# Optimization experiments

Measured on AMD Instinct MI355X. Metric: run time of the kernel, lower is better.

Reference implementation:

```python
import jax, jax.numpy as jnp
import numpy as np
import math

B, C, N, T = 16, 32, 500, 10
NH, DK = 8, 8
D = NH * DK  # 64
TT = 6       # tem_size after conv_temp1 (10->6)
EPS = 1e-5


def setup_inputs() -> dict:
    key = jax.random.key(0)
    ks = jax.random.split(key, 32)
    s = 0.05
    rn = lambda k, shp: jax.random.normal(k, shp, dtype=jnp.float32) * s
    return {
        "x": jax.random.normal(ks[0], (B, C, N, T), dtype=jnp.float32),
        "A": jax.random.uniform(ks[1], (N, N), dtype=jnp.float32) / N,
        "conv1_W": rn(ks[2], (32, 32)), "conv1_b": jnp.zeros((32,), jnp.float32),
        "te1_W": rn(ks[3], (64, 32)), "te1_b": jnp.zeros((64,), jnp.float32),
        "convq_W": rn(ks[4], (64, 64, 1, 3)), "convq_b": jnp.zeros((64,), jnp.float32),
        "convk_W": rn(ks[5], (64, 64, 1, 3)), "convk_b": jnp.zeros((64,), jnp.float32),
        "linv_W": rn(ks[6], (64, 64)), "linv_b": jnp.zeros((64,), jnp.float32),
        "lino_W": rn(ks[7], (64, 64)), "lino_b": jnp.zeros((64,), jnp.float32),
        "te2_W": rn(ks[8], (32, 64)), "te2_b": jnp.zeros((32,), jnp.float32),
        "mlp_W": rn(ks[9], (64, 160)), "mlp_b": jnp.zeros((64,), jnp.float32),
        "ct1_W": rn(ks[10], (6, 10)), "ct1_b": jnp.zeros((6,), jnp.float32),
        "tat_c1_W": rn(ks[11], (32,)), "tat_c2_W": rn(ks[12], (500,)),
        "tat_w": rn(ks[13], (500, 32)), "tat_b": jnp.zeros((6, 6), jnp.float32),
        "tat_v": rn(ks[14], (6, 6)),
        "bn1_g": jnp.ones((6,), jnp.float32), "bn1_b": jnp.zeros((6,), jnp.float32),
        "bn2_g": jnp.ones((32,), jnp.float32), "bn2_b": jnp.zeros((32,), jnp.float32),
    }


def _forward(x, A, conv1_W, conv1_b, te1_W, te1_b, convq_W, convq_b, convk_W, convk_b,
             linv_W, linv_b, lino_W, lino_b, te2_W, te2_b, mlp_W, mlp_b, ct1_W, ct1_b,
             tat_c1_W, tat_c2_W, tat_w, tat_b, tat_v, bn1_g, bn1_b, bn2_g, bn2_b):
    b, c, n, t = x.shape
    c1x1 = lambda z, W, bb: jnp.einsum('bchw,oc->bohw', z, W) + bb[None, :, None, None]
    residual = c1x1(x, conv1_W, conv1_b)                      # (B,32,N,T)
    h = c1x1(x, te1_W, te1_b)                                 # (B,64,N,T)
    # --- temporal-context multi-head self-attention (att bias is 0 in source due to bug) ---
    dn = ('NCHW', 'OIHW', 'NCHW')
    q = jax.lax.conv_general_dilated(h, convq_W, (1, 1), ((0, 0), (1, 1)), dimension_numbers=dn) + convq_b[None, :, None, None]
    k = jax.lax.conv_general_dilated(h, convk_W, (1, 1), ((0, 0), (1, 1)), dimension_numbers=dn) + convk_b[None, :, None, None]
    sh = lambda z: z.reshape(b, NH, DK, n, t).transpose(0, 3, 1, 4, 2)  # (B,N,h,T,dk)
    q, k = sh(q), sh(k)
    hp = h.transpose(0, 2, 3, 1)                              # (B,N,T,64)
    v = (hp @ linv_W.T + linv_b).reshape(b, n, t, NH, DK).transpose(0, 1, 3, 2, 4)
    p = jax.nn.softmax(jnp.einsum('bnhtd,bnhsd->bnhts', q, k) / math.sqrt(DK), axis=-1)
    o = jnp.einsum('bnhts,bnhsd->bnhtd', p, v).transpose(0, 1, 3, 2, 4).reshape(b, n, t, D)
    h = (o @ lino_W.T + lino_b).transpose(0, 3, 1, 2)         # (B,64,N,T)
    h = c1x1(h, te2_W, te2_b)                                 # (B,32,N,T)
    # --- multi_gcn_d: static adjacency diffusion + per-timestep attention adjacency ---
    co = h.shape[1]
    xt = h.transpose(0, 3, 2, 1)                              # (B,T,N,C)
    att = jax.nn.softmax(jnp.einsum('btnc,btmc->btnm', xt, xt) / math.sqrt(co), axis=-1)
    outs = [h]
    z = jnp.einsum('btvc,wv->btwc', xt, A); outs.append(z.transpose(0, 3, 2, 1))
    z = jnp.einsum('btvc,wv->btwc', z, A);  outs.append(z.transpose(0, 3, 2, 1))
    z = jnp.einsum('btvc,btwv->btwc', xt, att); outs.append(z.transpose(0, 3, 2, 1))
    z = jnp.einsum('btvc,btwv->btwc', z, att);  outs.append(z.transpose(0, 3, 2, 1))
    hc = c1x1(jnp.concatenate(outs, axis=1), mlp_W, mlp_b)    # (B,64,N,T)
    g = jnp.tanh(hc[:, :co]) * jax.nn.sigmoid(hc[:, co:])     # (B,32,N,10)
    # --- conv_temp1: 1x1 conv over the time axis, 10 -> 6 ---
    g = jnp.einsum('bcnt,st->bcns', g, ct1_W) + ct1_b[None, None, None, :]  # (B,32,N,6)
    # --- TATT_1 temporal attention coefficients ---
    f1 = jnp.einsum('bcnt,c->btn', g, tat_c1_W)               # (B,6,N)
    f2 = jnp.einsum('bcnt,n->bct', g, tat_c2_W)               # (B,32,6)
    logits = jax.nn.sigmoid(jnp.einsum('btn,nc,bcs->bts', f1, tat_w, f2) + tat_b)
    logits = jnp.einsum('pt,bts->bps', tat_v, logits)         # (B,6,6)
    lp = logits.transpose(0, 2, 1)
    mu = lp.mean((0, 2), keepdims=True); var = lp.var((0, 2), keepdims=True)
    lp = (lp - mu) / jnp.sqrt(var + EPS) * bn1_g[None, :, None] + bn1_b[None, :, None]
    coefs = jax.nn.softmax(lp.transpose(0, 2, 1), axis=-1)    # (B,6,6)
    Tc = coefs.transpose(0, 2, 1)
    xo = jnp.einsum('bcnl,blq->bcnq', g, Tc)                  # (B,32,N,6)
    xo = jnp.where(xo > 0, xo, 0.01 * xo) + residual[..., -xo.shape[-1]:]
    mu = xo.mean((0, 2, 3), keepdims=True); var = xo.var((0, 2, 3), keepdims=True)
    return (xo - mu) / jnp.sqrt(var + EPS) * bn2_g[None, :, None, None] + bn2_b[None, :, None, None]


def reference(x, A, conv1_W, conv1_b, te1_W, te1_b, convq_W, convq_b, convk_W, convk_b,
              linv_W, linv_b, lino_W, lino_b, te2_W, te2_b, mlp_W, mlp_b, ct1_W, ct1_b,
              tat_c1_W, tat_c2_W, tat_w, tat_b, tat_v, bn1_g, bn1_b, bn2_g, bn2_b):
    return _forward(x, A, conv1_W, conv1_b, te1_W, te1_b, convq_W, convq_b, convk_W, convk_b,
                    linv_W, linv_b, lino_W, lino_b, te2_W, te2_b, mlp_W, mlp_b, ct1_W, ct1_b,
                    tat_c1_W, tat_c2_W, tat_w, tat_b, tat_v, bn1_g, bn1_b, bn2_g, bn2_b)
```

## Files before the change

kernel.cpp:

```cpp
#include <hip/hip_runtime.h>

typedef unsigned short u16;
typedef unsigned int u32;

__device__ __forceinline__ float b2f(u16 v) { return __uint_as_float((u32)v << 16); }
__device__ __forceinline__ float lopart(u32 u) { return __uint_as_float(u << 16); }
__device__ __forceinline__ float hipart(u32 u) { return __uint_as_float(u & 0xffff0000u); }
__device__ __forceinline__ u16 f2b(float f) {
  u32 u = __float_as_uint(f);
  u32 r = u + 0x7fffu + ((u >> 16) & 1u);
  return (u16)(r >> 16);
}
__device__ __forceinline__ u32 pk2(float a, float b) {
  return (u32)f2b(a) | ((u32)f2b(b) << 16);
}
__device__ __forceinline__ u32 cvtpk(float lo, float hi) {
  u32 r;
  asm("v_cvt_pk_bf16_f32 %0, %1, %2" : "=v"(r) : "v"(lo), "v"(hi));
  return r;
}

struct Ptrs { const void* p[29]; };

typedef __attribute__((ext_vector_type(8))) short short8;
typedef __attribute__((ext_vector_type(4))) float floatx4;

__global__ void k_resolve(const void* __restrict__ g1, int* __restrict__ dtf) {
  if (threadIdx.x == 0) {
    u32 w = *(const u32*)g1;
    *dtf = ((w & 0xffffu) != 0) ? 1 : 0;
  }
}

__global__ __launch_bounds__(256) void k_cvt(Ptrs ps, const int* __restrict__ dtf,
                                             float* __restrict__ Wf) {
  bool BF = *dtf != 0;
  int j = blockIdx.x * 256 + threadIdx.x;
  if (j >= 65322) return;
  const int SZ[27] = {1024,32,2048,64,12288,64,12288,64,4096,64,4096,64,2048,32,
                      10240,64,60,6,32,500,16000,36,36,6,6,32,32};
  int t = 0, off = 0;
#pragma unroll
  for (int k = 0; k < 27; ++k) {
    if (t == k && j >= off + SZ[k]) { off += SZ[k]; t = k + 1; }
  }
  const void* src = ps.p[2 + t];
  int l = j - off;
  Wf[j] = BF ? b2f(((const u16*)src)[l]) : ((const float*)src)[l];
}

__global__ __launch_bounds__(256) void k_pk(const void* __restrict__ A, const int* __restrict__ dtf,
                                            u16* __restrict__ Abf) {
  bool BF = *dtf != 0;
  int i = blockIdx.x * 256 + threadIdx.x;
  if (i >= 262144) return;
  int r = i >> 9, v = i & 511;
  bool in = (r < 500) && (v < 500);
  u16 o = 0;
  if (in) o = BF ? ((const u16*)A)[r * 500 + v] : f2b(((const float*)A)[r * 500 + v]);
  Abf[i] = o;
}

__global__ __launch_bounds__(256, 4) void k_a2m(const u16* __restrict__ Abf,
                                                u16* __restrict__ A2bf) {
  __shared__ u32 blsT[8192];
  int tid = threadIdx.x;
  int c0 = blockIdx.x * 32;
  for (int i = tid; i < 8192; i += 256) {
    int c = i & 31, h = i >> 5;
    int r0 = 2 * h;
    u32 lo = Abf[r0 * 512 + c0 + c];
    u32 hi = Abf[(r0 + 1) * 512 + c0 + c];
    blsT[c * 256 + (((h & 0xFC) ^ ((c & 15) << 2)) | (h & 3))] = lo | (hi << 16);
  }
  __syncthreads();
  int lane = tid & 63, wave = tid >> 6;
  int q = lane >> 4, ln = lane & 15;
  int rbase = blockIdx.y * 64 + wave * 16;
  const u32* Au = (const u32*)Abf;
  int arow = (rbase + ln) * 256;
  union F8 { u32 u[4]; short8 s; };
  floatx4 acc[2] = {{0.f,0.f,0.f,0.f},{0.f,0.f,0.f,0.f}};
  for (int c2 = 0; c2 < 16; ++c2) {
    int hb = c2 * 16 + q * 4;
    F8 af;
#pragma unroll
    for (int i2 = 0; i2 < 4; ++i2) af.u[i2] = Au[arow + hb + i2];
#pragma unroll
    for (int t2 = 0; t2 < 2; ++t2) {
      int c = t2 * 16 + ln;
      int baseT = c * 256 + (hb ^ ((c & 15) << 2));
      F8 bf;
#pragma unroll
      for (int i2 = 0; i2 < 4; ++i2) bf.u[i2] = blsT[baseT + i2];
      acc[t2] = __builtin_amdgcn_mfma_f32_16x16x32_bf16(af.s, bf.s, acc[t2], 0, 0, 0);
    }
  }
#pragma unroll
  for (int t2 = 0; t2 < 2; ++t2) {
#pragma unroll
    for (int i2 = 0; i2 < 4; ++i2) {
      int r = rbase + q * 4 + i2;
      A2bf[r * 512 + c0 + t2 * 16 + ln] = f2b(acc[t2][i2]);
    }
  }
}

__global__ __launch_bounds__(256) void k_wprep(const float* __restrict__ Wf, float* __restrict__ WT,
                                               u16* __restrict__ WBu) {
  int i = blockIdx.x * 256 + threadIdx.x;
  if (i < 1024) {
    WT[i] = Wf[(i & 31) * 32 + (i >> 5)];
  } else if (i < 7168) {
    int j2 = i - 1024;
    int o = j2 & 63, ct = j2 >> 6;
    int c = ct / 3, tap = ct - c * 3;
    float sq = 0.f, sk = 0.f;
    for (int i2 = 0; i2 < 64; ++i2) {
      float te = Wf[1056 + i2 * 32 + c];
      sq += Wf[3168 + o * 192 + i2 * 3 + tap] * te;
      sk += Wf[15520 + o * 192 + i2 * 3 + tap] * te;
    }
    ((u32*)WT)[i] = pk2(sq, sk);
  } else if (i < 7552) {
    int j2 = i - 7168;
    int f = j2 >> 6, o = j2 & 63;
    int wbase = (f & 1) ? 15520 : 3168;
    float S0 = 0.f, S1 = 0.f, S2 = 0.f;
    for (int i2 = 0; i2 < 64; ++i2) {
      float tb = Wf[3104 + i2];
      S0 += Wf[wbase + o * 192 + i2 * 3 + 0] * tb;
      S1 += Wf[wbase + o * 192 + i2 * 3 + 1] * tb;
      S2 += Wf[wbase + o * 192 + i2 * 3 + 2] * tb;
    }
    float r;
    if (f == 0)      r = Wf[15456 + o] + S0 + S1 + S2;
    else if (f == 1) r = Wf[27808 + o] + S0 + S1 + S2;
    else if (f < 4)  r = S0;
    else             r = S2;
    WT[i] = r;
  } else if (i < 9600) {
    int j2 = i - 7552;
    int c = j2 >> 6, o = j2 & 63;
    float s = 0.f;
    for (int i2 = 0; i2 < 64; ++i2)
      s += Wf[27872 + o * 64 + i2] * Wf[1056 + i2 * 32 + c];
    WT[i] = s;
  } else if (i < 9664) {
    int o = i - 9600;
    float s = Wf[31968 + o];
    for (int i2 = 0; i2 < 64; ++i2)
      s += Wf[27872 + o * 64 + i2] * Wf[3104 + i2];
    WT[i] = s;
  } else if (i < 11712) {
    int j2 = i - 9664;
    int jj = j2 >> 5, c = j2 & 31;
    float s = 0.f;
    for (int o2 = 0; o2 < 64; ++o2)
      s += Wf[36192 + c * 64 + o2] * Wf[32032 + o2 * 64 + jj];
    WT[i] = s;
  } else if (i < 11744) {
    int c = i - 11712;
    float s = Wf[38240 + c];
    for (int o2 = 0; o2 < 64; ++o2)
      s += Wf[36192 + c * 64 + o2] * Wf[36128 + o2];
    WT[i] = s;
  } else if (i < 21984) {
    int j2 = i - 11744;
    int j = j2 & 7, lanev = (j2 >> 3) & 63, ct = (j2 >> 9) & 3, kt = j2 >> 11;
    int qv = lanev >> 4, lnv = lanev & 15;
    int o = ct * 16 + lnv, k = kt * 32 + qv * 8 + j;
    WBu[j2] = f2b(Wf[38272 + o * 160 + k]);
  }
}

__global__ __launch_bounds__(256, 5) void k_front3(
    const void* __restrict__ xraw, const int* __restrict__ dtf, const float* __restrict__ WT,
    const float* __restrict__ c1B,
    float* __restrict__ h3x, float* __restrict__ res6)
{
  __shared__ __align__(16) float arena[4][1920];
  int tid = threadIdx.x;
  int wave = tid >> 6, lane = tid & 63;
  float* Aw = arena[wave];
  int pair = blockIdx.x * 4 + wave;
  int b = pair / 500, n = pair - b * 500;

  const float* c1T  = WT;
  const u32*   qkF  = (const u32*)(WT + 1024);
  const float* bCq  = WT + 7168;
  const float* bCk  = WT + 7232;
  const float* bE0q = WT + 7296;
  const float* bE0k = WT + 7360;
  const float* bE2q = WT + 7424;
  const float* bE2k = WT + 7488;
  const float* vT   = WT + 7552;
  const float* bvp  = WT + 9600;
  const float* otT  = WT + 9664;
  const float* botp = WT + 11712;

  {
    bool BF = *dtf != 0;
    int c0 = lane >> 1, hf = (lane & 1) * 5;
    int base = ((b * 32 + c0) * 500 + n) * 10 + hf;
    float* dst = Aw + c0 * 12 + hf;
    if (BF) {
      const u16* xp = (const u16*)xraw + base;
#pragma unroll
      for (int k2 = 0; k2 < 5; ++k2) dst[k2] = b2f(xp[k2]);
    } else {
      const float* xp = (const float*)xraw + base;
#pragma unroll
      for (int k2 = 0; k2 < 5; ++k2) dst[k2] = xp[k2];
    }
  }
  __builtin_amdgcn_wave_barrier();

  int cl = lane & 31, th = lane >> 5;

  {
    float r0 = c1B[cl], r1 = r0, r2 = r0;
#pragma unroll 4
    for (int i = 0; i < 32; ++i) {
      float w = c1T[i * 32 + cl];
      const float* xr = Aw + i * 12 + 4 + th * 3;
      r0 += w * xr[0]; r1 += w * xr[1]; r2 += w * xr[2];
    }
    float* rp = res6 + ((b * 32 + cl) * 500 + n) * 6 + th * 3;
    rp[0] = r0; rp[1] = r1; rp[2] = r2;
  }

  float qr[10], kr[10], vr[10];
  {
    float cq = bCq[lane], ck = bCk[lane], bv = bvp[lane];
#pragma unroll
    for (int t = 0; t < 10; ++t) { qr[t] = cq; kr[t] = ck; vr[t] = bv; }
    qr[0] -= bE0q[lane]; kr[0] -= bE0k[lane];
    qr[9] -= bE2q[lane]; kr[9] -= bE2k[lane];
    const u32* qp0 = qkF + lane;
    const float* vp0 = vT + lane;
#pragma unroll 2
    for (int c = 0; c < 32; ++c) {
      const float* xr = Aw + c * 12;
      float4 ha = *(const float4*)xr;
      float4 hb = *(const float4*)(xr + 4);
      float2 hc = *(const float2*)(xr + 8);
      u32 u0 = qp0[c * 192];
      u32 u1 = qp0[c * 192 + 64];
      u32 u2 = qp0[c * 192 + 128];
      float wv = vp0[c * 64];
      float q0 = lopart(u0), q1 = lopart(u1), q2 = lopart(u2);
      float k0 = hipart(u0), k1 = hipart(u1), k2v = hipart(u2);
      float hh[10] = {ha.x, ha.y, ha.z, ha.w, hb.x, hb.y, hb.z, hb.w, hc.x, hc.y};
#pragma unroll
      for (int t = 0; t < 10; ++t) { float c_ = hh[t]; qr[t] += q1 * c_; kr[t] += k1 * c_; vr[t] += wv * c_; }
#pragma unroll
      for (int t = 1; t < 10; ++t) { float c_ = hh[t - 1]; qr[t] += q0 * c_; kr[t] += k0 * c_; }
#pragma unroll
      for (int t = 0; t < 9; ++t) { float c_ = hh[t + 1]; qr[t] += q2 * c_; kr[t] += k2v * c_; }
    }
  }
  __builtin_amdgcn_wave_barrier();
  {
    u32* qu = (u32*)Aw + lane * 5;
#pragma unroll
    for (int m = 0; m < 5; ++m) qu[m] = pk2(qr[2 * m], qr[2 * m + 1]);
    float* kp = Aw + 320 + lane * 12;
    *(float4*)kp       = make_float4(kr[0], kr[1], kr[2], kr[3]);
    *(float4*)(kp + 4) = make_float4(kr[4], kr[5], kr[6], kr[7]);
    *(float2*)(kp + 8) = make_float2(kr[8], kr[9]);
  }
  __builtin_amdgcn_wave_barrier();

  {
    const u32* qb = (const u32*)Aw;
#pragma unroll
    for (int pass = 0; pass < 2; ++pass) {
      int row = pass * 64 + lane;
      if (row < 80) {
        int h8 = (row / 10) * 8, r = row - (row / 10) * 10;
        int rm = r >> 1, rs = r & 1;
        float sv[10];
#pragma unroll
        for (int s = 0; s < 10; ++s) sv[s] = 0.f;
#pragma unroll 2
        for (int d = 0; d < 8; ++d) {
          int jj = h8 + d;
          u32 qu = qb[jj * 5 + rm];
          float qv = rs ? hipart(qu) : lopart(qu);
          const float* kp2 = Aw + 320 + jj * 12;
          float4 ka = *(const float4*)kp2;
          float4 kb = *(const float4*)(kp2 + 4);
          float2 kc = *(const float2*)(kp2 + 8);
          sv[0] += qv * ka.x; sv[1] += qv * ka.y; sv[2] += qv * ka.z; sv[3] += qv * ka.w;
          sv[4] += qv * kb.x; sv[5] += qv * kb.y; sv[6] += qv * kb.z; sv[7] += qv * kb.w;
          sv[8] += qv * kc.x; sv[9] += qv * kc.y;
        }
        const float sc_ = 0.35355339059327373f;
        float mx = sv[0];
#pragma unroll
        for (int s = 1; s < 10; ++s) mx = fmaxf(mx, sv[s]);
        float tot = 0.f, ev[10];
#pragma unroll
        for (int s = 0; s < 10; ++s) { ev[s] = expf((sv[s] - mx) * sc_); tot += ev[s]; }
        float inv = 1.f / tot;
        float* pp = Aw + 1088 + row * 10;
#pragma unroll
        for (int s = 0; s < 10; ++s) pp[s] = ev[s] * inv;
      }
    }
  }
  __builtin_amdgcn_wave_barrier();

  {
    const float* pb = Aw + 1088 + (lane >> 3) * 100;
    float orr[10];
#pragma unroll
    for (int t = 0; t < 10; ++t) {
      const float* pr = pb + t * 10;
      float a = 0.f;
#pragma unroll
      for (int s = 0; s < 10; ++s) a += pr[s] * vr[s];
      orr[t] = a;
    }
    float* op = Aw + lane * 12;
    *(float4*)op       = make_float4(orr[0], orr[1], orr[2], orr[3]);
    *(float4*)(op + 4) = make_float4(orr[4], orr[5], orr[6], orr[7]);
    *(float2*)(op + 8) = make_float2(orr[8], orr[9]);
  }
  __builtin_amdgcn_wave_barrier();

  {
    float bt2 = botp[cl];
    float a5[5];
#pragma unroll
    for (int k2 = 0; k2 < 5; ++k2) a5[k2] = bt2;
    const float* tp0 = otT + cl;
    const float* base = Aw + th * 5;
#pragma unroll 2
    for (int j = 0; j < 64; ++j) {
      float w = tp0[j * 32];
      const float* lp = base + j * 12;
#pragma unroll
      for (int k2 = 0; k2 < 5; ++k2) a5[k2] += w * lp[k2];
    }
    int t0 = th * 5;
#pragma unroll
    for (int k2 = 0; k2 < 5; ++k2)
      h3x[((b * 10 + t0 + k2) * 500 + n) * 32 + cl] = a5[k2];
  }
}

__global__ __launch_bounds__(256, 4) void k_z12m(const float* __restrict__ h3x,
    const u16* __restrict__ Abf, const u16* __restrict__ A2bf,
    float* __restrict__ z1x, float* __restrict__ z2x) {
  __shared__ u32 xlsT[8192];
  int tid = threadIdx.x, bt = blockIdx.x;
  const float* src = h3x + bt * 16000;
  for (int i = tid; i < 8192; i += 256) {
    int n = i & 31, h = i >> 5;
    int r0 = 2 * h;
    float v0 = (r0 < 500) ? src[r0 * 32 + n] : 0.f;
    float v1 = (r0 + 1 < 500) ? src[(r0 + 1) * 32 + n] : 0.f;
    xlsT[n * 256 + (((h & 0xFC) ^ ((n & 15) << 2)) | (h & 3))] = pk2(v0, v1);
  }
  __syncthreads();
  int lane = tid & 63, wave = tid >> 6;
  int q = lane >> 4, ln = lane & 15;
  int rbase = blockIdx.y * 64 + wave * 16;
  const u32* Au = (const u32*)Abf;
  const u32* A2u = (const u32*)A2bf;
  int arow = (rbase + ln) * 256;
  union F8 { u32 u[4]; short8 s; };
  floatx4 acc1[2] = {{0.f,0.f,0.f,0.f},{0.f,0.f,0.f,0.f}};
  floatx4 acc2[2] = {{0.f,0.f,0.f,0.f},{0.f,0.f,0.f,0.f}};
  for (int c2 = 0; c2 < 16; ++c2) {
    int hb = c2 * 16 + q * 4;
    F8 a1f, a2f;
#pragma unroll
    for (int i2 = 0; i2 < 4; ++i2) {
      a1f.u[i2] = Au[arow + hb + i2];
      a2f.u[i2] = A2u[arow + hb + i2];
    }
#pragma unroll
    for (int t2 = 0; t2 < 2; ++t2) {
      int n = t2 * 16 + ln;
      int baseT = n * 256 + (hb ^ ((n & 15) << 2));
      F8 bf;
#pragma unroll
      for (int i2 = 0; i2 < 4; ++i2) bf.u[i2] = xlsT[baseT + i2];
      acc1[t2] = __builtin_amdgcn_mfma_f32_16x16x32_bf16(a1f.s, bf.s, acc1[t2], 0, 0, 0);
      acc2[t2] = __builtin_amdgcn_mfma_f32_16x16x32_bf16(a2f.s, bf.s, acc2[t2], 0, 0, 0);
    }
  }
  int outb = bt * 16000;
#pragma unroll
  for (int t2 = 0; t2 < 2; ++t2) {
#pragma unroll
    for (int i2 = 0; i2 < 4; ++i2) {
      int r = rbase + q * 4 + i2;
      if (r < 500) {
        z1x[outb + r * 32 + t2 * 16 + ln] = acc1[t2][i2];
        z2x[outb + r * 32 + t2 * 16 + ln] = acc2[t2][i2];
      }
    }
  }
}

__global__ __launch_bounds__(256, 2) void k_attn2(const float* __restrict__ keys,
                                                  const float* __restrict__ vals,
                                                  float* __restrict__ outp) {
  __shared__ u32 xls[8192];
  __shared__ u32 pch[4][272];
  int tid = threadIdx.x, bt = blockIdx.x;
  const float* kb = keys + bt * 16000;
  const float* vb = vals + bt * 16000;
  for (int i = tid; i < 8192; i += 256) {
    int r = i >> 4, cu = i & 15;
    u32 u = 0;
    if (r < 500) {
      float2 g = *(const float2*)(kb + r * 32 + cu * 2);
      u = pk2(g.x, g.y);
    }
    xls[(r << 4) | (cu ^ (r & 15))] = u;
  }
  __syncthreads();
  int lane = tid & 63, wave = tid >> 6;
  int q = lane >> 4, ln = lane & 15;
  int rbase = blockIdx.y * 64 + wave * 16;
  union F8 { u32 u[4]; short8 s; };
  F8 af;
  {
    int r = rbase + ln;
#pragma unroll
    for (int i2 = 0; i2 < 4; ++i2)
      af.u[i2] = xls[(r << 4) | ((q * 4 + i2) ^ (r & 15))];
  }
  floatx4 acc[32];
#pragma unroll
  for (int ct = 0; ct < 32; ++ct) {
    int r2 = ct * 16 + ln;
    F8 bf;
#pragma unroll
    for (int i2 = 0; i2 < 4; ++i2)
      bf.u[i2] = xls[(r2 << 4) | ((q * 4 + i2) ^ (r2 & 15))];
    acc[ct] = __builtin_amdgcn_mfma_f32_16x16x32_bf16(af.s, bf.s,
              (floatx4){0.f, 0.f, 0.f, 0.f}, 0, 0, 0);
  }
  if (ln >= 4) {
#pragma unroll
    for (int i2 = 0; i2 < 4; ++i2) acc[31][i2] = -1e30f;
  }
  const float sc = 0.17677669529663687f;
  float inv[4];
#pragma unroll
  for (int i2 = 0; i2 < 4; ++i2) {
    float m = -1e30f;
#pragma unroll
    for (int ct = 0; ct < 32; ++ct) m = fmaxf(m, acc[ct][i2]);
#pragma unroll
    for (int d = 1; d < 16; d <<= 1) m = fmaxf(m, __shfl_xor(m, d));
    float s = 0.f;
#pragma unroll
    for (int ct = 0; ct < 32; ++ct) {
      float e = expf((acc[ct][i2] - m) * sc);
      acc[ct][i2] = e; s += e;
    }
#pragma unroll
    for (int d = 1; d < 16; d <<= 1) s += __shfl_xor(s, d);
    inv[i2] = 1.f / s;
  }
  __syncthreads();
  for (int i = tid; i < 8192; i += 256) {
    int n = i & 31, h = i >> 5;
    int r0 = 2 * h;
    float v0 = (r0 < 500) ? vb[r0 * 32 + n] : 0.f;
    float v1 = (r0 + 1 < 500) ? vb[(r0 + 1) * 32 + n] : 0.f;
    xls[n * 256 + (((h & 0xFC) ^ ((n & 15) << 2)) | (h & 3))] = pk2(v0, v1);
  }
  __syncthreads();
  floatx4 zacc[2] = {{0.f,0.f,0.f,0.f},{0.f,0.f,0.f,0.f}};
  u32* myp = pch[wave];
  u16* pw = (u16*)myp;
  for (int c2 = 0; c2 < 16; ++c2) {
#pragma unroll
    for (int t2 = 0; t2 < 2; ++t2) {
      int ct = c2 * 2 + t2;
#pragma unroll
      for (int i2 = 0; i2 < 4; ++i2)
        pw[(q * 4 + i2) * 34 + t2 * 16 + ln] = f2b(acc[ct][i2] * inv[i2]);
    }
    __builtin_amdgcn_wave_barrier();
    F8 pa;
#pragma unroll
    for (int i2 = 0; i2 < 4; ++i2) pa.u[i2] = myp[ln * 17 + q * 4 + i2];
    int hb = c2 * 16 + q * 4;
#pragma unroll
    for (int t2 = 0; t2 < 2; ++t2) {
      int n = t2 * 16 + ln;
      int baseT = n * 256 + (hb ^ ((n & 15) << 2));
      F8 bf;
#pragma unroll
      for (int i2 = 0; i2 < 4; ++i2) bf.u[i2] = xls[baseT + i2];
      zacc[t2] = __builtin_amdgcn_mfma_f32_16x16x32_bf16(pa.s, bf.s, zacc[t2], 0, 0, 0);
    }
    __builtin_amdgcn_wave_barrier();
  }
  int outb = bt * 16000;
#pragma unroll
  for (int t2 = 0; t2 < 2; ++t2) {
#pragma unroll
    for (int i2 = 0; i2 < 4; ++i2) {
      int r = rbase + q * 4 + i2;
      if (r < 500) outp[outb + r * 32 + t2 * 16 + ln] = zacc[t2][i2];
    }
  }
}

__global__ __launch_bounds__(256, 2) void k_gate(
    const float* __restrict__ h3x, const float* __restrict__ z1x, const float* __restrict__ z2x,
    const float* __restrict__ z3x, const float* __restrict__ z4x,
    const u32* __restrict__ WBq, const float* __restrict__ mlpB,
    const float* __restrict__ ct1W, const float* __restrict__ ct1B,
    float* __restrict__ g2w)
{
  __shared__ u32 wlds[5120];
  int tid = threadIdx.x;
  for (int i = tid; i < 5120; i += 256) wlds[i] = WBq[i];
  __syncthreads();
  int lane = tid & 63, wave = tid >> 6;
  int q = lane >> 4, ln = lane & 15;
  int b = blockIdx.y;
  int n0 = blockIdx.x * 32 + wave * 8;
  int nA = n0 + (ln & 7);
  int tAb = ln >> 3;
  int nD = n0 + (q & 1) * 4;
  int tDb = q >> 1;
  float g2a[4][2][6];
#pragma unroll
  for (int i = 0; i < 4; ++i)
#pragma unroll
    for (int ch = 0; ch < 2; ++ch)
#pragma unroll
      for (int s = 0; s < 6; ++s) g2a[i][ch][s] = 0.f;
  float bias[4];
#pragma unroll
  for (int ct = 0; ct < 4; ++ct) bias[ct] = mlpB[ct * 16 + ln];
  union F8 { u32 u[4]; short8 s; };
  for (int tile = 0; tile < 5; ++tile) {
    int tA = tile * 2 + tAb;
    int offA = (((b * 10 + tA) * 500) + nA) * 32 + q * 8;
    floatx4 acc[4];
#pragma unroll
    for (int ct = 0; ct < 4; ++ct) acc[ct] = (floatx4){bias[ct], bias[ct], bias[ct], bias[ct]};
#pragma unroll
    for (int kt = 0; kt < 5; ++kt) {
      const float* sp = kt == 0 ? h3x : kt == 1 ? z1x : kt == 2 ? z2x : kt == 3 ? z3x : z4x;
      float4 a0 = *(const float4*)(sp + offA);
      float4 a1 = *(const float4*)(sp + offA + 4);
      F8 af;
      af.u[0] = cvtpk(a0.x, a0.y);
      af.u[1] = cvtpk(a0.z, a0.w);
      af.u[2] = cvtpk(a1.x, a1.y);
      af.u[3] = cvtpk(a1.z, a1.w);
#pragma unroll
      for (int ct = 0; ct < 4; ++ct) {
        F8 bfr;
        const u32* wp = wlds + (((kt * 4 + ct) << 6) + lane) * 4;
#pragma unroll
        for (int i2 = 0; i2 < 4; ++i2) bfr.u[i2] = wp[i2];
        acc[ct] = __builtin_amdgcn_mfma_f32_16x16x32_bf16(af.s, bfr.s, acc[ct], 0, 0, 0);
      }
    }
    int tD = tile * 2 + tDb;
    float c6[6];
#pragma unroll
    for (int s = 0; s < 6; ++s) c6[s] = ct1W[s * 10 + tD];
#pragma unroll
    for (int i = 0; i < 4; ++i) {
      float e0 = __expf(2.f * acc[0][i]);
      float g0 = ((e0 - 1.f) / (e0 + 1.f)) * (1.f / (1.f + __expf(-acc[2][i])));
      float e1 = __expf(2.f * acc[1][i]);
      float g1 = ((e1 - 1.f) / (e1 + 1.f)) * (1.f / (1.f + __expf(-acc[3][i])));
#pragma unroll
      for (int s = 0; s < 6; ++s) {
        g2a[i][0][s] += g0 * c6[s];
        g2a[i][1][s] += g1 * c6[s];
      }
    }
  }
#pragma unroll
  for (int i = 0; i < 4; ++i)
#pragma unroll
    for (int ch = 0; ch < 2; ++ch)
#pragma unroll
      for (int s = 0; s < 6; ++s)
        g2a[i][ch][s] += __shfl_xor(g2a[i][ch][s], 32);
  if (q < 2) {
#pragma unroll
    for (int i = 0; i < 4; ++i) {
      int n = nD + i;
      if (n < 500) {
#pragma unroll
        for (int ch = 0; ch < 2; ++ch) {
          int c = ln + ch * 16;
          float* gp = g2w + ((b * 32 + c) * 500 + n) * 6;
#pragma unroll
          for (int s = 0; s < 6; ++s) gp[s] = g2a[i][ch][s] + ct1B[s];
        }
      }
    }
  }
}

__global__ __launch_bounds__(256) void k_f1n(const float* __restrict__ g2w,
                                             const float* __restrict__ tc1W,
                                             float* __restrict__ f1w) {
  int i = blockIdx.x * 256 + threadIdx.x;
  if (i >= 48000) return;
  int b = i / 3000, rem = i - b * 3000, s = rem / 500, n = rem - s * 500;
  float a = 0.f;
  for (int c = 0; c < 32; ++c) a += g2w[((b * 32 + c) * 500 + n) * 6 + s] * tc1W[c];
  f1w[(b * 6 + s) * 500 + n] = a;
}

__global__ __launch_bounds__(64) void k_f2(const float* __restrict__ g2w,
                                           const float* __restrict__ c2W, float* __restrict__ f2w) {
  int b = blockIdx.x >> 5, c = blockIdx.x & 31, lane = threadIdx.x;
  float acc[6];
#pragma unroll
  for (int t = 0; t < 6; ++t) acc[t] = 0.f;
  for (int n = lane; n < 500; n += 64) {
    float w = c2W[n];
    const float* gp = g2w + ((b * 32 + c) * 500 + n) * 6;
#pragma unroll
    for (int t = 0; t < 6; ++t) acc[t] += w * gp[t];
  }
#pragma unroll
  for (int t = 0; t < 6; ++t)
    for (int off = 32; off; off >>= 1) acc[t] += __shfl_xor(acc[t], off);
  if (lane == 0) {
#pragma unroll
    for (int t = 0; t < 6; ++t) f2w[(b * 32 + c) * 6 + t] = acc[t];
  }
}

__global__ __launch_bounds__(256) void k_tatt(
    const float* __restrict__ f1w, const float* __restrict__ tatw,
    const float* __restrict__ f2w, const float* __restrict__ tatb, const float* __restrict__ tatv,
    float* __restrict__ lg2w)
{
  __shared__ float mid[192];
  __shared__ float lgt[36];
  int b = blockIdx.x, tid = threadIdx.x;
  if (tid < 192) {
    int t = tid >> 5, c = tid & 31;
    float a = 0.f;
    const float* f1p = f1w + (b * 6 + t) * 500;
    for (int n = 0; n < 500; ++n) a += f1p[n] * tatw[n * 32 + c];
    mid[t * 32 + c] = a;
  }
  __syncthreads();
  if (tid < 36) {
    int t = tid / 6, s = tid - t * 6;
    float a = tatb[t * 6 + s];
    for (int c = 0; c < 32; ++c) a += mid[t * 32 + c] * f2w[(b * 32 + c) * 6 + s];
    lgt[t * 6 + s] = 1.f / (1.f + expf(-a));
  }
  __syncthreads();
  if (tid < 36) {
    int p = tid / 6, s = tid - p * 6;
    float a = 0.f;
#pragma unroll
    for (int t2 = 0; t2 < 6; ++t2) a += tatv[p * 6 + t2] * lgt[t2 * 6 + s];
    lg2w[(b * 6 + p) * 6 + s] = a;
  }
}

__global__ __launch_bounds__(128) void k_coefs(const float* __restrict__ lg2w,
    const float* __restrict__ bn1g, const float* __restrict__ bn1b, float* __restrict__ tcw) {
  __shared__ float mu[6], iv[6], gg[6], bb[6];
  int tid = threadIdx.x;
  if (tid < 6) {
    float s = 0.f, sq = 0.f;
    for (int b = 0; b < 16; ++b)
      for (int q = 0; q < 6; ++q) {
        float v = lg2w[(b * 6 + q) * 6 + tid];
        s += v; sq += v * v;
      }
    float m = s / 96.f;
    mu[tid] = m;
    iv[tid] = rsqrtf(sq / 96.f - m * m + 1e-5f);
    gg[tid] = bn1g[tid]; bb[tid] = bn1b[tid];
  }
  __syncthreads();
  for (int idx = tid; idx < 96; idx += 128) {
    int b = idx / 6, q = idx - b * 6;
    float v[6], mx = -1e30f;
#pragma unroll
    for (int l = 0; l < 6; ++l) {
      v[l] = (lg2w[(b * 6 + q) * 6 + l] - mu[l]) * iv[l] * gg[l] + bb[l];
      mx = fmaxf(mx, v[l]);
    }
    float tot = 0.f;
#pragma unroll
    for (int l = 0; l < 6; ++l) { v[l] = expf(v[l] - mx); tot += v[l]; }
    float inv = 1.f / tot;
#pragma unroll
    for (int l = 0; l < 6; ++l) tcw[(b * 6 + l) * 6 + q] = v[l] * inv;
  }
}

__global__ __launch_bounds__(256) void k_xo(const float* __restrict__ g2w,
    const float* __restrict__ res6, const float* __restrict__ tcw,
    float* __restrict__ xow, float* __restrict__ stats) {
  __shared__ float Tcl[36];
  __shared__ float redS[32][8], redQ[32][8];
  int b = blockIdx.x, chunk = blockIdx.y, tid = threadIdx.x;
  if (tid < 36) Tcl[tid] = tcw[b * 36 + tid];
  __syncthreads();
  int c = tid & 31, sub = tid >> 5;
  int n0 = chunk * 50;
  float s = 0.f, sq = 0.f;
  for (int idx = sub; idx < 300; idx += 8) {
    int nl = idx / 6, q = idx - nl * 6;
    int n = n0 + nl;
    int base = ((b * 32 + c) * 500 + n) * 6;
    const float* gp = g2w + base;
    float xv = 0.f;
#pragma unroll
    for (int l = 0; l < 6; ++l) xv += gp[l] * Tcl[l * 6 + q];
    xv = xv > 0.f ? xv : 0.01f * xv;
    xv += res6[base + q];
    xow[base + q] = xv;
    s += xv; sq += xv * xv;
  }
  redS[c][sub] = s; redQ[c][sub] = sq;
  __syncthreads();
  if (sub == 0) {
    float ts = 0.f, tq = 0.f;
#pragma unroll
    for (int k = 0; k < 8; ++k) { ts += redS[c][k]; tq += redQ[c][k]; }
    atomicAdd(&stats[c], ts);
    atomicAdd(&stats[32 + c], tq);
  }
}

__global__ __launch_bounds__(256) void k_out(const float* __restrict__ xow,
    const float* __restrict__ stats, const float* __restrict__ g2c, const float* __restrict__ b2c,
    float* __restrict__ out) {
  int base = (blockIdx.x * 256 + threadIdx.x) * 4;
#pragma unroll
  for (int k = 0; k < 4; ++k) {
    int i = base + k;
    int c = (i / 3000) & 31;
    float m = stats[c] * (1.f / 48000.f);
    float var = stats[32 + c] * (1.f / 48000.f) - m * m;
    out[i] = (xow[i] - m) * rsqrtf(var + 1e-5f) * g2c[c] + b2c[c];
  }
}

extern "C" void kernel_launch(void* const* d_in, const int* in_sizes, int n_in,
                              void* d_out, int out_size, void* d_ws, size_t ws_size,
                              hipStream_t stream)
{
  (void)in_sizes; (void)out_size;

  float* ws = (float*)d_ws;
  float* Af   = ws;
  float* Wf   = Af + 250000;
  float* A2   = Wf + 65536;
  float* h3x  = A2 + 250000;
  float* z1x  = h3x + 2560000;
  float* z2x  = z1x + 2560000;
  float* z3x  = z2x + 2560000;
  float* z4x  = z3x + 2560000;
  float* res6 = z4x + 2560000;
  float* g2w  = res6 + 1536000;
  float* f1w  = g2w + 1536000;
  float* f2w  = f1w + 48000;
  float* lg2w = f2w + 3072;
  float* tcw  = lg2w + 576;
  float* stats= tcw + 576;
  int*   dtf  = (int*)(stats + 64);
  float* xow  = z1x;
  u16*   Abf  = (u16*)g2w;
  u16*   A2bf = (u16*)(g2w + 131072);
  float* WTp  = g2w + 262144;
  u16*   WBu  = (u16*)f1w;
  if (ws_size < (size_t)16489952 * sizeof(float)) return;

  const float* c1B  = Wf + 1024;
  const float* mlpB = Wf + 48512;
  const float* ct1W = Wf + 48576;
  const float* ct1B = Wf + 48636;
  const float* tc1W = Wf + 48642;
  const float* tc2W = Wf + 48674;
  const float* tatw = Wf + 49174;
  const float* tatb = Wf + 65174;
  const float* tatv = Wf + 65210;
  const float* bn1g = Wf + 65246;
  const float* bn1b = Wf + 65252;
  const float* bn2g = Wf + 65258;
  const float* bn2b = Wf + 65290;

  Ptrs ps;
  for (int i = 0; i < 29; ++i) ps.p[i] = (i < n_in) ? d_in[i] : d_in[0];

  hipMemsetAsync(stats, 0, 64 * sizeof(float), stream);
  k_resolve<<<dim3(1),     64, 0, stream>>>(ps.p[25], dtf);
  k_cvt  <<<dim3(256),     256, 0, stream>>>(ps, dtf, Wf);
  k_wprep<<<dim3(86),      256, 0, stream>>>(Wf, WTp, WBu);
  k_pk   <<<dim3(1024),    256, 0, stream>>>(ps.p[1], dtf, Abf);
  k_a2m  <<<dim3(16, 8),   256, 0, stream>>>(Abf, A2bf);
  k_front3<<<dim3(2000),   256, 0, stream>>>(ps.p[0], dtf, WTp, c1B, h3x, res6);
  k_z12m <<<dim3(160, 8),  256, 0, stream>>>(h3x, Abf, A2bf, z1x, z2x);
  k_attn2<<<dim3(160, 8),  256, 0, stream>>>(h3x, h3x, z3x);
  k_attn2<<<dim3(160, 8),  256, 0, stream>>>(h3x, z3x, z4x);
  k_gate <<<dim3(16, 16),  256, 0, stream>>>(h3x, z1x, z2x, z3x, z4x,
                                             (const u32*)WBu, mlpB, ct1W, ct1B, g2w);
  k_f1n  <<<dim3(188),     256, 0, stream>>>(g2w, tc1W, f1w);
  k_f2   <<<dim3(512),      64, 0, stream>>>(g2w, tc2W, f2w);
  k_tatt <<<dim3(16),      256, 0, stream>>>(f1w, tatw, f2w, tatb, tatv, lg2w);
  k_coefs<<<dim3(1),       128, 0, stream>>>(lg2w, bn1g, bn1b, tcw);
  k_xo   <<<dim3(16, 10),  256, 0, stream>>>(g2w, res6, tcw, xow, stats);
  k_out  <<<dim3(1500),    256, 0, stream>>>(xow, stats, bn2g, bn2b, (float*)d_out);
}
```

Before: 467.6 us.

## Split attention key columns across wave pairs with cross-wave softmax reduction

Each k_attn2 block now handles 32 query rows instead of 64, and two waves share each 16-row tile, each covering half of the 512 key columns. The partial row max and row sum are exchanged through shared memory, normalization is deferred to the final output, and the two partial PV accumulators are summed through LDS. This halves the per-thread accumulator registers so three blocks per CU can be resident, and it doubles the grid. The cost is that each block reloads the full key and value tiles for half as many rows, so global loading and LDS packing are duplicated, and it adds extra barriers and uses the faster __expf.

```diff
diff --git a/kernel.cpp b/kernel.cpp
--- a/kernel.cpp
+++ b/kernel.cpp
@@ -407,11 +407,11 @@
   }
 }
 
-__global__ __launch_bounds__(256, 2) void k_attn2(const float* __restrict__ keys,
+__global__ __launch_bounds__(256, 3) void k_attn2(const float* __restrict__ keys,
                                                   const float* __restrict__ vals,
                                                   float* __restrict__ outp) {
   __shared__ u32 xls[8192];
-  __shared__ u32 pch[4][272];
+  __shared__ u32 aux[1280];
   int tid = threadIdx.x, bt = blockIdx.x;
   const float* kb = keys + bt * 16000;
   const float* vb = vals + bt * 16000;
@@ -427,7 +427,12 @@
   __syncthreads();
   int lane = tid & 63, wave = tid >> 6;
   int q = lane >> 4, ln = lane & 15;
-  int rbase = blockIdx.y * 64 + wave * 16;
+  int wrow = wave >> 1, ch = wave & 1;
+  int rbase = blockIdx.y * 32 + wrow * 16;
+  float* smx = (float*)aux;
+  float* sms = smx + 64;
+  u32* myp = aux + 128 + wave * 272;
+  float* zex = (float*)aux;
   union F8 { u32 u[4]; short8 s; };
   F8 af;
   {
@@ -436,41 +441,55 @@
     for (int i2 = 0; i2 < 4; ++i2)
       af.u[i2] = xls[(r << 4) | ((q * 4 + i2) ^ (r & 15))];
   }
-  floatx4 acc[32];
-#pragma unroll
-  for (int ct = 0; ct < 32; ++ct) {
-    int r2 = ct * 16 + ln;
+  floatx4 acc[16];
+#pragma unroll
+  for (int ctl = 0; ctl < 16; ++ctl) {
+    int r2 = (ch * 16 + ctl) * 16 + ln;
     F8 bf;
 #pragma unroll
     for (int i2 = 0; i2 < 4; ++i2)
       bf.u[i2] = xls[(r2 << 4) | ((q * 4 + i2) ^ (r2 & 15))];
-    acc[ct] = __builtin_amdgcn_mfma_f32_16x16x32_bf16(af.s, bf.s,
+    acc[ctl] = __builtin_amdgcn_mfma_f32_16x16x32_bf16(af.s, bf.s,
               (floatx4){0.f, 0.f, 0.f, 0.f}, 0, 0, 0);
   }
-  if (ln >= 4) {
-#pragma unroll
-    for (int i2 = 0; i2 < 4; ++i2) acc[31][i2] = -1e30f;
+  if (ch == 1 && ln >= 4) {
+#pragma unroll
+    for (int i2 = 0; i2 < 4; ++i2) acc[15][i2] = -1e30f;
   }
   const float sc = 0.17677669529663687f;
-  float inv[4];
+  float m[4];
 #pragma unroll
   for (int i2 = 0; i2 < 4; ++i2) {
-    float m = -1e30f;
-#pragma unroll
-    for (int ct = 0; ct < 32; ++ct) m = fmaxf(m, acc[ct][i2]);
-#pragma unroll
-    for (int d = 1; d < 16; d <<= 1) m = fmaxf(m, __shfl_xor(m, d));
+    float mm = -1e30f;
+#pragma unroll
+    for (int ctl = 0; ctl < 16; ++ctl) mm = fmaxf(mm, acc[ctl][i2]);
+#pragma unroll
+    for (int d = 1; d < 16; d <<= 1) mm = fmaxf(mm, __shfl_xor(mm, d));
+    m[i2] = mm;
+  }
+  if (ln == 0) {
+#pragma unroll
+    for (int i2 = 0; i2 < 4; ++i2) smx[wave * 16 + q * 4 + i2] = m[i2];
+  }
+  __syncthreads();
+  float sp[4];
+#pragma unroll
+  for (int i2 = 0; i2 < 4; ++i2) {
+    float mm = fmaxf(m[i2], smx[(wave ^ 1) * 16 + q * 4 + i2]);
     float s = 0.f;
 #pragma unroll
-    for (int ct = 0; ct < 32; ++ct) {
-      float e = expf((acc[ct][i2] - m) * sc);
-      acc[ct][i2] = e; s += e;
+    for (int ctl = 0; ctl < 16; ++ctl) {
+      float e = __expf((acc[ctl][i2] - mm) * sc);
+      acc[ctl][i2] = e; s += e;
     }
 #pragma unroll
     for (int d = 1; d < 16; d <<= 1) s += __shfl_xor(s, d);
-    inv[i2] = 1.f / s;
-  }
-  __syncthreads();
+    sp[i2] = s;
+  }
+  if (ln == 0) {
+#pragma unroll
+    for (int i2 = 0; i2 < 4; ++i2) sms[wave * 16 + q * 4 + i2] = sp[i2];
+  }
   for (int i = tid; i < 8192; i += 256) {
     int n = i & 31, h = i >> 5;
     int r0 = 2 * h;
@@ -479,22 +498,25 @@
     xls[n * 256 + (((h & 0xFC) ^ ((n & 15) << 2)) | (h & 3))] = pk2(v0, v1);
   }
   __syncthreads();
+  float inv[4];
+#pragma unroll
+  for (int i2 = 0; i2 < 4; ++i2)
+    inv[i2] = 1.f / (sp[i2] + sms[(wave ^ 1) * 16 + q * 4 + i2]);
   floatx4 zacc[2] = {{0.f,0.f,0.f,0.f},{0.f,0.f,0.f,0.f}};
-  u32* myp = pch[wave];
   u16* pw = (u16*)myp;
-  for (int c2 = 0; c2 < 16; ++c2) {
+  for (int c2l = 0; c2l < 8; ++c2l) {
 #pragma unroll
     for (int t2 = 0; t2 < 2; ++t2) {
-      int ct = c2 * 2 + t2;
+      int ctl = c2l * 2 + t2;
 #pragma unroll
       for (int i2 = 0; i2 < 4; ++i2)
-        pw[(q * 4 + i2) * 34 + t2 * 16 + ln] = f2b(acc[ct][i2] * inv[i2]);
+        pw[(q * 4 + i2) * 34 + t2 * 16 + ln] = f2b(acc[ctl][i2]);
     }
     __builtin_amdgcn_wave_barrier();
     F8 pa;
 #pragma unroll
     for (int i2 = 0; i2 < 4; ++i2) pa.u[i2] = myp[ln * 17 + q * 4 + i2];
-    int hb = c2 * 16 + q * 4;
+    int hb = (ch * 8 + c2l) * 16 + q * 4;
 #pragma unroll
     for (int t2 = 0; t2 < 2; ++t2) {
       int n = t2 * 16 + ln;
@@ -506,13 +528,27 @@
     }
     __builtin_amdgcn_wave_barrier();
   }
-  int outb = bt * 16000;
-#pragma unroll
-  for (int t2 = 0; t2 < 2; ++t2) {
-#pragma unroll
-    for (int i2 = 0; i2 < 4; ++i2) {
-      int r = rbase + q * 4 + i2;
-      if (r < 500) outp[outb + r * 32 + t2 * 16 + ln] = zacc[t2][i2];
+  __syncthreads();
+  if (ch) {
+#pragma unroll
+    for (int t2 = 0; t2 < 2; ++t2)
+#pragma unroll
+      for (int i2 = 0; i2 < 4; ++i2)
+        zex[wrow * 544 + (q * 4 + i2) * 34 + t2 * 16 + ln] = zacc[t2][i2];
+  }
+  __syncthreads();
+  if (!ch) {
+    int outb = bt * 16000;
+#pragma unroll
+    for (int t2 = 0; t2 < 2; ++t2) {
+#pragma unroll
+      for (int i2 = 0; i2 < 4; ++i2) {
+        int r = rbase + q * 4 + i2;
+        if (r < 500) {
+          float vsum = zacc[t2][i2] + zex[wrow * 544 + (q * 4 + i2) * 34 + t2 * 16 + ln];
+          outp[outb + r * 32 + t2 * 16 + ln] = vsum * inv[i2];
+        }
+      }
     }
   }
 }
@@ -815,8 +851,8 @@
   k_a2m  <<<dim3(16, 8),   256, 0, stream>>>(Abf, A2bf);
   k_front3<<<dim3(2000),   256, 0, stream>>>(ps.p[0], dtf, WTp, c1B, h3x, res6);
   k_z12m <<<dim3(160, 8),  256, 0, stream>>>(h3x, Abf, A2bf, z1x, z2x);
-  k_attn2<<<dim3(160, 8),  256, 0, stream>>>(h3x, h3x, z3x);
-  k_attn2<<<dim3(160, 8),  256, 0, stream>>>(h3x, z3x, z4x);
+  k_attn2<<<dim3(160, 16), 256, 0, stream>>>(h3x, h3x, z3x);
+  k_attn2<<<dim3(160, 16), 256, 0, stream>>>(h3x, z3x, z4x);
   k_gate <<<dim3(16, 16),  256, 0, stream>>>(h3x, z1x, z2x, z3x, z4x,
                                              (const u32*)WBu, mlpB, ct1W, ct1B, g2w);
   k_f1n  <<<dim3(188),     256, 0, stream>>>(g2w, tc1W, f1w);
```

New measurement: 441.8 us. 5.5% less time.
